# Kernel tuning notes

Measured on AMD Instinct MI355X. Metric: run time of the kernel, lower is better.

The kernel has to match this reference:

```python
import jax, jax.numpy as jnp
import numpy as np

B, SQ, SK, D, DV = 16, 2048, 2048, 64, 64
DROPOUT_P = 0.1


def setup_inputs() -> dict:
    key = jax.random.key(0)
    k1, k2, k3, k4 = jax.random.split(key, 4)
    return {
        "query": jax.random.normal(k1, (B, SQ, D), dtype=jnp.float32),
        "key": jax.random.normal(k2, (B, SK, D), dtype=jnp.float32),
        "value": jax.random.normal(k3, (B, SK, DV), dtype=jnp.float32),
        "drop_mask": jax.random.uniform(k4, (B, SQ, SK), dtype=jnp.float32),
    }


def reference(query, key, value, drop_mask):
    # scaled dot-product attention with explicit score matrix, as in the module
    scale = jnp.sqrt(jnp.asarray(key.shape[-1], dtype=query.dtype))
    qk = jnp.einsum("bqd,bkd->bqk", query, key) / scale  # [B, SQ, SK]
    attn = jax.nn.softmax(qk, axis=-1)
    # dropout: keep where uniform > p, rescale by 1/(1-p)
    keep = (drop_mask > DROPOUT_P).astype(attn.dtype)
    attn = attn * keep / (1.0 - DROPOUT_P)
    return jnp.einsum("bqk,bkv->bqv", attn, value)  # [B, SQ, DV]
```

## Files before the change

kernel.cpp:

```cpp
#include <hip/hip_runtime.h>
#include <hip/hip_bf16.h>

#define B_ 16
#define SQ_ 2048
#define SK_ 2048
#define D_ 64
#define DV_ 64
#define INV_KEEP 1.1111111f
#define QSCALE 0.1803368801f

typedef float f4 __attribute__((ext_vector_type(4)));
typedef __bf16 bf16x2 __attribute__((ext_vector_type(2)));
typedef __bf16 bf16x8 __attribute__((ext_vector_type(8)));
typedef short s16x4 __attribute__((ext_vector_type(4)));
typedef unsigned int u32;
typedef unsigned int u32x2 __attribute__((ext_vector_type(2)));
typedef unsigned int u32x4 __attribute__((ext_vector_type(4)));

static __device__ __forceinline__ unsigned short bf16u(float f) {
    u32 u = __builtin_bit_cast(u32, f);
    u += 0x7fffu + ((u >> 16) & 1u);
    return (unsigned short)(u >> 16);
}
static __device__ __forceinline__ u32 pk2(float lo, float hi) {
    return (u32)bf16u(lo) | ((u32)bf16u(hi) << 16);
}
static __device__ __forceinline__ u32 pkc(float lo, float hi) {
    bf16x2 t = {(__bf16)lo, (__bf16)hi};
    return __builtin_bit_cast(u32, t);
}

static __device__ __forceinline__ float fexp2(float x) {
#if __has_builtin(__builtin_amdgcn_exp2f)
    return __builtin_amdgcn_exp2f(x);
#else
    return exp2f(x);
#endif
}

static __device__ __forceinline__ void gload16(const void* g, void* l) {
    __builtin_amdgcn_global_load_lds(
        (const __attribute__((address_space(1))) unsigned int*)g,
        (__attribute__((address_space(3))) unsigned int*)l, 16, 0, 0);
}

template <int OFF>
static __device__ __forceinline__ f4 gload_f4(const float* p) {
    f4 d;
    if constexpr (OFF == 0)
        asm volatile("global_load_dwordx4 %0, %1, off" : "=v"(d) : "v"(p));
    else
        asm volatile("global_load_dwordx4 %0, %1, off offset:%2" : "=v"(d) : "v"(p), "i"(OFF));
    return d;
}

static __device__ __forceinline__ f4 mfma16(s16x4 a, s16x4 b, f4 c) {
#if __has_builtin(__builtin_amdgcn_mfma_f32_16x16x16bf16_1k)
    return __builtin_amdgcn_mfma_f32_16x16x16bf16_1k(a, b, c, 0, 0, 0);
#else
    f4 d;
    asm("v_mfma_f32_16x16x16_bf16 %0, %1, %2, %3" : "=v"(d) : "v"(a), "v"(b), "v"(c));
    return d;
#endif
}

__global__ __launch_bounds__(256) void kv_retile(const float* __restrict__ K,
                                                 const float* __restrict__ V,
                                                 unsigned short* __restrict__ KbT,
                                                 unsigned short* __restrict__ VtT) {
    if (blockIdx.x < 1024) {
        int b = blockIdx.x >> 6, kt = blockIdx.x & 63;
        int p = threadIdx.x;
        int s = p >> 6, g = (p >> 4) & 3, c = p & 15;
        int t = s & 1, h = s >> 1;
        const float* src = K + ((size_t)(b * SK_ + kt * 32 + 16 * t + c)) * D_ + 32 * h + 8 * g;
        f4 a = *(const f4*)src;
        f4 b2 = *(const f4*)(src + 4);
        u32x4 w;
        w[0] = pk2(a.x, a.y); w[1] = pk2(a.z, a.w);
        w[2] = pk2(b2.x, b2.y); w[3] = pk2(b2.z, b2.w);
        *(u32x4*)(KbT + ((size_t)(b * 64 + kt)) * 2048 + (size_t)p * 8) = w;
    } else {
        __shared__ float vt[32][65];
        int id = blockIdx.x - 1024;
        int b = id >> 6, kt = id & 63;
        int tid = threadIdx.x;
#pragma unroll
        for (int e = 0; e < 2; ++e) {
            int f = tid * 2 + e;
            int row = f >> 4, c4 = (f & 15) * 4;
            *(f4*)&vt[row][c4] = *(const f4*)(V + ((size_t)(b * SK_ + kt * 32 + row)) * DV_ + c4);
        }
        __syncthreads();
        int vb = tid >> 6, g = (tid >> 4) & 3, c = tid & 15;
        int v = vb * 16 + c;
        u32x4 w;
        w[0] = pk2(vt[4 * g + 0][v], vt[4 * g + 1][v]);
        w[1] = pk2(vt[4 * g + 2][v], vt[4 * g + 3][v]);
        w[2] = pk2(vt[16 + 4 * g + 0][v], vt[16 + 4 * g + 1][v]);
        w[3] = pk2(vt[16 + 4 * g + 2][v], vt[16 + 4 * g + 3][v]);
        *(u32x4*)(VtT + ((size_t)(b * 64 + kt)) * 2048 + (size_t)tid * 8) = w;
    }
}

template <int SPLIT>
__global__ __launch_bounds__(256) void attn_main(const float* __restrict__ Q,
                                                 const unsigned short* __restrict__ KbT,
                                                 const unsigned short* __restrict__ VtT,
                                                 const float* __restrict__ mask,
                                                 float* __restrict__ out,
                                                 float* __restrict__ accP,
                                                 float* __restrict__ lP) {
    constexpr int NT32 = SK_ / SPLIT / 32;
    constexpr int NB = 512 * SPLIT;
    __shared__ unsigned short sK[4][2048];
    __shared__ unsigned short sV[4][2048];

    int bswz = (blockIdx.x & 7) * (NB / 8) + (blockIdx.x >> 3);
    int wid  = threadIdx.x >> 6;
    int split = bswz & (SPLIT - 1);
    int strip = (bswz / SPLIT) * 4 + wid;
    int b  = strip >> 7;
    int q0 = (strip & 127) << 4;
    int kb = split * (SK_ / SPLIT);
    int lane = threadIdx.x & 63;
    int g = lane >> 4, c = lane & 15;

    const size_t tile0 = ((size_t)b * 64 + split * NT32) * 2048;
    const unsigned short* ksrc = KbT + tile0 + (size_t)threadIdx.x * 8;
    const unsigned short* vsrc = VtT + tile0 + (size_t)threadIdx.x * 8;
    const float* msrc = mask + ((size_t)(b * SQ_ + q0 + c)) * SK_ + kb + 4 * g;

    bf16x8 qf[2];
    {
        const float* qp = Q + ((size_t)(b * SQ_ + q0 + c)) * D_ + 8 * g;
#pragma unroll
        for (int h = 0; h < 2; ++h) {
            f4 a  = *(const f4*)(qp + h * 32);
            f4 bq = *(const f4*)(qp + h * 32 + 4);
            u32x4 wq;
            wq[0] = pk2(a.x * QSCALE, a.y * QSCALE);
            wq[1] = pk2(a.z * QSCALE, a.w * QSCALE);
            wq[2] = pk2(bq.x * QSCALE, bq.y * QSCALE);
            wq[3] = pk2(bq.z * QSCALE, bq.w * QSCALE);
            qf[h] = __builtin_bit_cast(bf16x8, wq);
        }
    }

    f4 mreg[4][2];

    auto kvload = [&](int dst, int srct) {
        gload16(ksrc + (size_t)srct * 2048, &sK[dst][wid * 512]);
        gload16(vsrc + (size_t)srct * 2048, &sV[dst][wid * 512]);
    };
    auto mload = [&](int dst, int srct) {
        const float* mp = msrc + (size_t)srct * 32;
        mreg[dst][0] = gload_f4<0>(mp);
        mreg[dst][1] = gload_f4<64>(mp);
    };

    mload(0, 0);
    kvload(0, 0); mload(1, 1);
    kvload(1, 1); mload(2, 2);
    kvload(2, 2); mload(3, 3);

    f4 acc[4];
#pragma unroll
    for (int vb = 0; vb < 4; ++vb) acc[vb] = (f4){0.f, 0.f, 0.f, 0.f};
    f4 ls0 = (f4){0.f, 0.f, 0.f, 0.f}, ls1 = (f4){0.f, 0.f, 0.f, 0.f};

    const unsigned short* kbL = &sK[0][0] + lane * 8;
    const unsigned short* vbL = &sV[0][0] + lane * 8;

#pragma unroll 4
    for (int kt = 0; kt < NT32; ++kt) {
        asm volatile("s_waitcnt vmcnt(10)" ::: "memory");
        __builtin_amdgcn_s_barrier();
        __builtin_amdgcn_sched_barrier(0);

        const int bi = kt & 3;
        const unsigned short* kB = kbL + bi * 2048;
        const unsigned short* vB = vbL + bi * 2048;

        u32x4 ka0 = *(const u32x4*)(kB);
        u32x4 ka1 = *(const u32x4*)(kB + 1024);
        u32x4 kc0 = *(const u32x4*)(kB + 512);
        u32x4 kc1 = *(const u32x4*)(kB + 1536);
        f4 st0 = (f4){0.f, 0.f, 0.f, 0.f}, st1 = (f4){0.f, 0.f, 0.f, 0.f};
        st0 = __builtin_amdgcn_mfma_f32_16x16x32_bf16(__builtin_bit_cast(bf16x8, ka0), qf[0], st0, 0, 0, 0);
        st0 = __builtin_amdgcn_mfma_f32_16x16x32_bf16(__builtin_bit_cast(bf16x8, ka1), qf[1], st0, 0, 0, 0);
        st1 = __builtin_amdgcn_mfma_f32_16x16x32_bf16(__builtin_bit_cast(bf16x8, kc0), qf[0], st1, 0, 0, 0);
        st1 = __builtin_amdgcn_mfma_f32_16x16x32_bf16(__builtin_bit_cast(bf16x8, kc1), qf[1], st1, 0, 0, 0);

        const f4 mk0 = mreg[bi][0], mk1 = mreg[bi][1];
        float pd0[4], pd1[4];
#pragma unroll
        for (int r = 0; r < 4; ++r) {
            float p0 = fexp2(st0[r]);
            ls0[r] += p0;
            pd0[r] = (mk0[r] > 0.1f) ? p0 : 0.f;
            float p1 = fexp2(st1[r]);
            ls1[r] += p1;
            pd1[r] = (mk1[r] > 0.1f) ? p1 : 0.f;
        }

        u32x2 pw0, pw1;
        pw0[0] = pkc(pd0[0], pd0[1]); pw0[1] = pkc(pd0[2], pd0[3]);
        pw1[0] = pkc(pd1[0], pd1[1]); pw1[1] = pkc(pd1[2], pd1[3]);
        s16x4 pb0 = __builtin_bit_cast(s16x4, pw0);
        s16x4 pb1 = __builtin_bit_cast(s16x4, pw1);
#pragma unroll
        for (int vb = 0; vb < 4; ++vb) {
            u32x4 vv = *(const u32x4*)(vB + vb * 512);
            u32x2 vlo, vhi;
            vlo[0] = vv[0]; vlo[1] = vv[1];
            vhi[0] = vv[2]; vhi[1] = vv[3];
            acc[vb] = mfma16(__builtin_bit_cast(s16x4, vlo), pb0, acc[vb]);
            acc[vb] = mfma16(__builtin_bit_cast(s16x4, vhi), pb1, acc[vb]);
        }

        __builtin_amdgcn_s_barrier();
        kvload((kt + 3) & 3, (kt + 3 < NT32) ? kt + 3 : NT32 - 1);
        mload((kt + 4) & 3, (kt + 4 < NT32) ? kt + 4 : NT32 - 1);
    }
    asm volatile("s_waitcnt vmcnt(0)" ::: "memory");

    float lf = ls0[0] + ls0[1] + ls0[2] + ls0[3] + ls1[0] + ls1[1] + ls1[2] + ls1[3];
    lf += __shfl_xor(lf, 16);
    lf += __shfl_xor(lf, 32);

    if constexpr (SPLIT == 1) {
        float li = INV_KEEP / lf;
        float* op = out + ((size_t)(b * SQ_ + q0 + c)) * DV_;
#pragma unroll
        for (int vb = 0; vb < 4; ++vb) {
            f4 o = acc[vb] * li;
            __builtin_nontemporal_store(o, (f4*)(op + 16 * vb + 4 * g));
        }
    } else {
        float* ap = accP + (((size_t)strip * SPLIT + split) * 64 + lane) * 16;
#pragma unroll
        for (int vb = 0; vb < 4; ++vb)
            *(f4*)(ap + 4 * vb) = acc[vb];
        if (g == 0)
            lP[((size_t)strip * SPLIT + split) * 16 + c] = lf;
    }
}

__global__ __launch_bounds__(256) void attn_combine2(const float* __restrict__ accP,
                                                     const float* __restrict__ lP,
                                                     float* __restrict__ out) {
    __shared__ float sacc[2 * 1280];
    __shared__ float sl[32];
    int strip = blockIdx.x;
    int t = threadIdx.x;
    const float* src = accP + (size_t)strip * 2048;
#pragma unroll
    for (int s = 0; s < 2; ++s)
        *(f4*)&sacc[s * 1280 + (t >> 2) * 20 + (t & 3) * 4] = *(const f4*)(src + s * 1024 + t * 4);
    if (t < 32) sl[t] = lP[(size_t)strip * 32 + t];
    __syncthreads();

    int q = t >> 4, j = t & 15;
    float L = sl[q] + sl[16 + q];
    float inv = INV_KEEP / L;
    int base = (16 * (j & 3) + q) * 20 + 4 * (j >> 2);
    f4 o = *(const f4*)&sacc[base] + *(const f4*)&sacc[1280 + base];
    o *= inv;
    int b  = strip >> 7;
    int q0 = (strip & 127) << 4;
    __builtin_nontemporal_store(o, (f4*)(out + ((size_t)(b * SQ_ + q0 + q)) * DV_ + 4 * j));
}

extern "C" void kernel_launch(void* const* d_in, const int* in_sizes, int n_in,
                              void* d_out, int out_size, void* d_ws, size_t ws_size,
                              hipStream_t stream) {
    const float* Q = (const float*)d_in[0];
    const float* K = (const float*)d_in[1];
    const float* V = (const float*)d_in[2];
    const float* M = (const float*)d_in[3];
    float* out = (float*)d_out;

    char* ws = (char*)d_ws;
    unsigned short* KbT  = (unsigned short*)ws;
    unsigned short* VtT  = (unsigned short*)(ws + (size_t)4 * 1024 * 1024);
    float*          accP = (float*)         (ws + (size_t)8 * 1024 * 1024);
    float*          lP   = (float*)         (ws + (size_t)24 * 1024 * 1024);

    const size_t need_split = (size_t)24 * 1024 * 1024 + (size_t)2048 * 2 * 16 * 4;

    kv_retile<<<2048, 256, 0, stream>>>(K, V, KbT, VtT);
    if (ws_size >= need_split) {
        attn_main<2><<<1024, 256, 0, stream>>>(Q, KbT, VtT, M, out, accP, lP);
        attn_combine2<<<2048, 256, 0, stream>>>(accP, lP, out);
    } else {
        attn_main<1><<<512, 256, 0, stream>>>(Q, KbT, VtT, M, out, nullptr, nullptr);
    }
}
```

Measured before the change: 91.25 us.

## Load K/V tiles directly into registers instead of shared LDS staging

Removes the shared-memory K/V ring buffer and the block-wide barriers. Each wave now loads its own K and V tile data straight into registers with a two-slot double buffer and a mask prefetch three tiles ahead. This drops the LDS round trip and the inter-wave synchronisation. In exchange, each of the four waves fetches the same K/V data separately, so global/L2 traffic for K/V is quadrupled and register pressure rises.

```diff
diff --git a/kernel.cpp b/kernel.cpp
--- a/kernel.cpp
+++ b/kernel.cpp
@@ -38,15 +38,18 @@
 #endif
 }
 
-static __device__ __forceinline__ void gload16(const void* g, void* l) {
-    __builtin_amdgcn_global_load_lds(
-        (const __attribute__((address_space(1))) unsigned int*)g,
-        (__attribute__((address_space(3))) unsigned int*)l, 16, 0, 0);
-}
-
 template <int OFF>
 static __device__ __forceinline__ f4 gload_f4(const float* p) {
     f4 d;
+    if constexpr (OFF == 0)
+        asm volatile("global_load_dwordx4 %0, %1, off" : "=v"(d) : "v"(p));
+    else
+        asm volatile("global_load_dwordx4 %0, %1, off offset:%2" : "=v"(d) : "v"(p), "i"(OFF));
+    return d;
+}
+template <int OFF>
+static __device__ __forceinline__ u32x4 gload_u4(const unsigned short* p) {
+    u32x4 d;
     if constexpr (OFF == 0)
         asm volatile("global_load_dwordx4 %0, %1, off" : "=v"(d) : "v"(p));
     else
@@ -113,8 +116,6 @@
                                                  float* __restrict__ lP) {
     constexpr int NT32 = SK_ / SPLIT / 32;
     constexpr int NB = 512 * SPLIT;
-    __shared__ unsigned short sK[4][2048];
-    __shared__ unsigned short sV[4][2048];
 
     int bswz = (blockIdx.x & 7) * (NB / 8) + (blockIdx.x >> 3);
     int wid  = threadIdx.x >> 6;
@@ -127,8 +128,8 @@
     int g = lane >> 4, c = lane & 15;
 
     const size_t tile0 = ((size_t)b * 64 + split * NT32) * 2048;
-    const unsigned short* ksrc = KbT + tile0 + (size_t)threadIdx.x * 8;
-    const unsigned short* vsrc = VtT + tile0 + (size_t)threadIdx.x * 8;
+    const unsigned short* ksrc = KbT + tile0 + (size_t)lane * 8;
+    const unsigned short* vsrc = VtT + tile0 + (size_t)lane * 8;
     const float* msrc = mask + ((size_t)(b * SQ_ + q0 + c)) * SK_ + kb + 4 * g;
 
     bf16x8 qf[2];
@@ -146,53 +147,56 @@
             qf[h] = __builtin_bit_cast(bf16x8, wq);
         }
     }
-
-    f4 mreg[4][2];
-
-    auto kvload = [&](int dst, int srct) {
-        gload16(ksrc + (size_t)srct * 2048, &sK[dst][wid * 512]);
-        gload16(vsrc + (size_t)srct * 2048, &sV[dst][wid * 512]);
+    __builtin_amdgcn_sched_barrier(0);
+
+    u32x4 kr[2][4];
+    u32x4 vr[2][4];
+    f4    mr[4][2];
+
+    auto kvload = [&](int slot, int srct) {
+        const unsigned short* kp = ksrc + (size_t)srct * 2048;
+        kr[slot][0] = gload_u4<0>(kp);
+        kr[slot][1] = gload_u4<1024>(kp);
+        kr[slot][2] = gload_u4<2048>(kp);
+        kr[slot][3] = gload_u4<3072>(kp);
+        const unsigned short* vp = vsrc + (size_t)srct * 2048;
+        vr[slot][0] = gload_u4<0>(vp);
+        vr[slot][1] = gload_u4<1024>(vp);
+        vr[slot][2] = gload_u4<2048>(vp);
+        vr[slot][3] = gload_u4<3072>(vp);
     };
-    auto mload = [&](int dst, int srct) {
+    auto mload = [&](int slot, int srct) {
         const float* mp = msrc + (size_t)srct * 32;
-        mreg[dst][0] = gload_f4<0>(mp);
-        mreg[dst][1] = gload_f4<64>(mp);
+        mr[slot][0] = gload_f4<0>(mp);
+        mr[slot][1] = gload_f4<64>(mp);
     };
 
     mload(0, 0);
-    kvload(0, 0); mload(1, 1);
-    kvload(1, 1); mload(2, 2);
-    kvload(2, 2); mload(3, 3);
+    mload(1, 1);
+    kvload(0, 0);
+    mload(2, 2);
 
     f4 acc[4];
 #pragma unroll
     for (int vb = 0; vb < 4; ++vb) acc[vb] = (f4){0.f, 0.f, 0.f, 0.f};
     f4 ls0 = (f4){0.f, 0.f, 0.f, 0.f}, ls1 = (f4){0.f, 0.f, 0.f, 0.f};
 
-    const unsigned short* kbL = &sK[0][0] + lane * 8;
-    const unsigned short* vbL = &sV[0][0] + lane * 8;
-
 #pragma unroll 4
     for (int kt = 0; kt < NT32; ++kt) {
-        asm volatile("s_waitcnt vmcnt(10)" ::: "memory");
-        __builtin_amdgcn_s_barrier();
+        kvload((kt + 1) & 1, (kt + 1 < NT32) ? kt + 1 : NT32 - 1);
+        mload((kt + 3) & 3, (kt + 3 < NT32) ? kt + 3 : NT32 - 1);
+        asm volatile("s_waitcnt vmcnt(12)" ::: "memory");
         __builtin_amdgcn_sched_barrier(0);
 
-        const int bi = kt & 3;
-        const unsigned short* kB = kbL + bi * 2048;
-        const unsigned short* vB = vbL + bi * 2048;
-
-        u32x4 ka0 = *(const u32x4*)(kB);
-        u32x4 ka1 = *(const u32x4*)(kB + 1024);
-        u32x4 kc0 = *(const u32x4*)(kB + 512);
-        u32x4 kc1 = *(const u32x4*)(kB + 1536);
+        const int ks = kt & 1, ms = kt & 3;
+
         f4 st0 = (f4){0.f, 0.f, 0.f, 0.f}, st1 = (f4){0.f, 0.f, 0.f, 0.f};
-        st0 = __builtin_amdgcn_mfma_f32_16x16x32_bf16(__builtin_bit_cast(bf16x8, ka0), qf[0], st0, 0, 0, 0);
-        st0 = __builtin_amdgcn_mfma_f32_16x16x32_bf16(__builtin_bit_cast(bf16x8, ka1), qf[1], st0, 0, 0, 0);
-        st1 = __builtin_amdgcn_mfma_f32_16x16x32_bf16(__builtin_bit_cast(bf16x8, kc0), qf[0], st1, 0, 0, 0);
-        st1 = __builtin_amdgcn_mfma_f32_16x16x32_bf16(__builtin_bit_cast(bf16x8, kc1), qf[1], st1, 0, 0, 0);
-
-        const f4 mk0 = mreg[bi][0], mk1 = mreg[bi][1];
+        st0 = __builtin_amdgcn_mfma_f32_16x16x32_bf16(__builtin_bit_cast(bf16x8, kr[ks][0]), qf[0], st0, 0, 0, 0);
+        st0 = __builtin_amdgcn_mfma_f32_16x16x32_bf16(__builtin_bit_cast(bf16x8, kr[ks][2]), qf[1], st0, 0, 0, 0);
+        st1 = __builtin_amdgcn_mfma_f32_16x16x32_bf16(__builtin_bit_cast(bf16x8, kr[ks][1]), qf[0], st1, 0, 0, 0);
+        st1 = __builtin_amdgcn_mfma_f32_16x16x32_bf16(__builtin_bit_cast(bf16x8, kr[ks][3]), qf[1], st1, 0, 0, 0);
+
+        const f4 mk0 = mr[ms][0], mk1 = mr[ms][1];
         float pd0[4], pd1[4];
 #pragma unroll
         for (int r = 0; r < 4; ++r) {
@@ -211,19 +215,16 @@
         s16x4 pb1 = __builtin_bit_cast(s16x4, pw1);
 #pragma unroll
         for (int vb = 0; vb < 4; ++vb) {
-            u32x4 vv = *(const u32x4*)(vB + vb * 512);
+            u32x4 vv = vr[ks][vb];
             u32x2 vlo, vhi;
             vlo[0] = vv[0]; vlo[1] = vv[1];
             vhi[0] = vv[2]; vhi[1] = vv[3];
             acc[vb] = mfma16(__builtin_bit_cast(s16x4, vlo), pb0, acc[vb]);
             acc[vb] = mfma16(__builtin_bit_cast(s16x4, vhi), pb1, acc[vb]);
         }
-
-        __builtin_amdgcn_s_barrier();
-        kvload((kt + 3) & 3, (kt + 3 < NT32) ? kt + 3 : NT32 - 1);
-        mload((kt + 4) & 3, (kt + 4 < NT32) ? kt + 4 : NT32 - 1);
     }
     asm volatile("s_waitcnt vmcnt(0)" ::: "memory");
+    __builtin_amdgcn_sched_barrier(0);
 
     float lf = ls0[0] + ls0[1] + ls0[2] + ls0[3] + ls1[0] + ls1[1] + ls1[2] + ls1[3];
     lf += __shfl_xor(lf, 16);
```

New measurement: 105.4 us. +15.5%, slower.

## Split keys four ways with a shallower pipeline to raise occupancy

Applied to the files above, without the earlier changes.

Moves from a 2-way to a 4-way key split (2048 blocks) and adds a combine kernel that sums four partials. LDS ring buffers shrink from 4 to 2 stages and the mask prefetch shrinks from 4 register sets to one, with launch_bounds(256,7) added so more waves fit per CU. The goal is more latency hiding through more resident waves and blocks. The cost is less prefetch depth for the mask stream, which dominates memory traffic, plus twice the partial-accumulator traffic and a heavier combine step.

```diff
diff --git a/kernel.cpp b/kernel.cpp
--- a/kernel.cpp
+++ b/kernel.cpp
@@ -29,7 +29,6 @@
     bf16x2 t = {(__bf16)lo, (__bf16)hi};
     return __builtin_bit_cast(u32, t);
 }
-
 static __device__ __forceinline__ float fexp2(float x) {
 #if __has_builtin(__builtin_amdgcn_exp2f)
     return __builtin_amdgcn_exp2f(x);
@@ -37,13 +36,11 @@
     return exp2f(x);
 #endif
 }
-
 static __device__ __forceinline__ void gload16(const void* g, void* l) {
     __builtin_amdgcn_global_load_lds(
         (const __attribute__((address_space(1))) unsigned int*)g,
         (__attribute__((address_space(3))) unsigned int*)l, 16, 0, 0);
 }
-
 template <int OFF>
 static __device__ __forceinline__ f4 gload_f4(const float* p) {
     f4 d;
@@ -53,7 +50,6 @@
         asm volatile("global_load_dwordx4 %0, %1, off offset:%2" : "=v"(d) : "v"(p), "i"(OFF));
     return d;
 }
-
 static __device__ __forceinline__ f4 mfma16(s16x4 a, s16x4 b, f4 c) {
 #if __has_builtin(__builtin_amdgcn_mfma_f32_16x16x16bf16_1k)
     return __builtin_amdgcn_mfma_f32_16x16x16bf16_1k(a, b, c, 0, 0, 0);
@@ -104,17 +100,17 @@
 }
 
 template <int SPLIT>
-__global__ __launch_bounds__(256) void attn_main(const float* __restrict__ Q,
-                                                 const unsigned short* __restrict__ KbT,
-                                                 const unsigned short* __restrict__ VtT,
-                                                 const float* __restrict__ mask,
-                                                 float* __restrict__ out,
-                                                 float* __restrict__ accP,
-                                                 float* __restrict__ lP) {
+__global__ __launch_bounds__(256, 7) void attn_main(const float* __restrict__ Q,
+                                                    const unsigned short* __restrict__ KbT,
+                                                    const unsigned short* __restrict__ VtT,
+                                                    const float* __restrict__ mask,
+                                                    float* __restrict__ out,
+                                                    float* __restrict__ accP,
+                                                    float* __restrict__ lP) {
     constexpr int NT32 = SK_ / SPLIT / 32;
     constexpr int NB = 512 * SPLIT;
-    __shared__ unsigned short sK[4][2048];
-    __shared__ unsigned short sV[4][2048];
+    __shared__ unsigned short sK[2][2048];
+    __shared__ unsigned short sV[2][2048];
 
     int bswz = (blockIdx.x & 7) * (NB / 8) + (blockIdx.x >> 3);
     int wid  = threadIdx.x >> 6;
@@ -146,62 +142,66 @@
             qf[h] = __builtin_bit_cast(bf16x8, wq);
         }
     }
-
-    f4 mreg[4][2];
+    __builtin_amdgcn_sched_barrier(0);
 
     auto kvload = [&](int dst, int srct) {
         gload16(ksrc + (size_t)srct * 2048, &sK[dst][wid * 512]);
         gload16(vsrc + (size_t)srct * 2048, &sV[dst][wid * 512]);
     };
-    auto mload = [&](int dst, int srct) {
-        const float* mp = msrc + (size_t)srct * 32;
-        mreg[dst][0] = gload_f4<0>(mp);
-        mreg[dst][1] = gload_f4<64>(mp);
-    };
-
-    mload(0, 0);
-    kvload(0, 0); mload(1, 1);
-    kvload(1, 1); mload(2, 2);
-    kvload(2, 2); mload(3, 3);
+
+    f4 mka, mkb;
+    mka = gload_f4<0>(msrc);
+    mkb = gload_f4<64>(msrc);
+    kvload(0, 0);
+    kvload(1, 1);
 
     f4 acc[4];
 #pragma unroll
     for (int vb = 0; vb < 4; ++vb) acc[vb] = (f4){0.f, 0.f, 0.f, 0.f};
-    f4 ls0 = (f4){0.f, 0.f, 0.f, 0.f}, ls1 = (f4){0.f, 0.f, 0.f, 0.f};
+    float lf = 0.f;
 
     const unsigned short* kbL = &sK[0][0] + lane * 8;
     const unsigned short* vbL = &sV[0][0] + lane * 8;
 
 #pragma unroll 4
     for (int kt = 0; kt < NT32; ++kt) {
-        asm volatile("s_waitcnt vmcnt(10)" ::: "memory");
+        asm volatile("s_waitcnt vmcnt(2)" ::: "memory");
         __builtin_amdgcn_s_barrier();
         __builtin_amdgcn_sched_barrier(0);
 
-        const int bi = kt & 3;
+        const int bi = kt & 1;
         const unsigned short* kB = kbL + bi * 2048;
         const unsigned short* vB = vbL + bi * 2048;
 
-        u32x4 ka0 = *(const u32x4*)(kB);
-        u32x4 ka1 = *(const u32x4*)(kB + 1024);
-        u32x4 kc0 = *(const u32x4*)(kB + 512);
-        u32x4 kc1 = *(const u32x4*)(kB + 1536);
         f4 st0 = (f4){0.f, 0.f, 0.f, 0.f}, st1 = (f4){0.f, 0.f, 0.f, 0.f};
-        st0 = __builtin_amdgcn_mfma_f32_16x16x32_bf16(__builtin_bit_cast(bf16x8, ka0), qf[0], st0, 0, 0, 0);
-        st0 = __builtin_amdgcn_mfma_f32_16x16x32_bf16(__builtin_bit_cast(bf16x8, ka1), qf[1], st0, 0, 0, 0);
-        st1 = __builtin_amdgcn_mfma_f32_16x16x32_bf16(__builtin_bit_cast(bf16x8, kc0), qf[0], st1, 0, 0, 0);
-        st1 = __builtin_amdgcn_mfma_f32_16x16x32_bf16(__builtin_bit_cast(bf16x8, kc1), qf[1], st1, 0, 0, 0);
-
-        const f4 mk0 = mreg[bi][0], mk1 = mreg[bi][1];
+        {
+            u32x4 ka = *(const u32x4*)(kB);
+            u32x4 kc = *(const u32x4*)(kB + 512);
+            st0 = __builtin_amdgcn_mfma_f32_16x16x32_bf16(__builtin_bit_cast(bf16x8, ka), qf[0], st0, 0, 0, 0);
+            st1 = __builtin_amdgcn_mfma_f32_16x16x32_bf16(__builtin_bit_cast(bf16x8, kc), qf[0], st1, 0, 0, 0);
+        }
+        {
+            u32x4 ka = *(const u32x4*)(kB + 1024);
+            u32x4 kc = *(const u32x4*)(kB + 1536);
+            st0 = __builtin_amdgcn_mfma_f32_16x16x32_bf16(__builtin_bit_cast(bf16x8, ka), qf[1], st0, 0, 0, 0);
+            st1 = __builtin_amdgcn_mfma_f32_16x16x32_bf16(__builtin_bit_cast(bf16x8, kc), qf[1], st1, 0, 0, 0);
+        }
+
         float pd0[4], pd1[4];
 #pragma unroll
         for (int r = 0; r < 4; ++r) {
             float p0 = fexp2(st0[r]);
-            ls0[r] += p0;
-            pd0[r] = (mk0[r] > 0.1f) ? p0 : 0.f;
+            lf += p0;
+            pd0[r] = (mka[r] > 0.1f) ? p0 : 0.f;
             float p1 = fexp2(st1[r]);
-            ls1[r] += p1;
-            pd1[r] = (mk1[r] > 0.1f) ? p1 : 0.f;
+            lf += p1;
+            pd1[r] = (mkb[r] > 0.1f) ? p1 : 0.f;
+        }
+
+        {
+            const float* mp = msrc + (size_t)((kt + 1 < NT32) ? kt + 1 : NT32 - 1) * 32;
+            mka = gload_f4<0>(mp);
+            mkb = gload_f4<64>(mp);
         }
 
         u32x2 pw0, pw1;
@@ -220,12 +220,12 @@
         }
 
         __builtin_amdgcn_s_barrier();
-        kvload((kt + 3) & 3, (kt + 3 < NT32) ? kt + 3 : NT32 - 1);
-        mload((kt + 4) & 3, (kt + 4 < NT32) ? kt + 4 : NT32 - 1);
+        __builtin_amdgcn_sched_barrier(0);
+        kvload(bi, (kt + 2 < NT32) ? kt + 2 : NT32 - 1);
     }
     asm volatile("s_waitcnt vmcnt(0)" ::: "memory");
-
-    float lf = ls0[0] + ls0[1] + ls0[2] + ls0[3] + ls1[0] + ls1[1] + ls1[2] + ls1[3];
+    __builtin_amdgcn_sched_barrier(0);
+
     lf += __shfl_xor(lf, 16);
     lf += __shfl_xor(lf, 32);
 
@@ -247,25 +247,28 @@
     }
 }
 
-__global__ __launch_bounds__(256) void attn_combine2(const float* __restrict__ accP,
+__global__ __launch_bounds__(256) void attn_combine4(const float* __restrict__ accP,
                                                      const float* __restrict__ lP,
                                                      float* __restrict__ out) {
-    __shared__ float sacc[2 * 1280];
-    __shared__ float sl[32];
+    __shared__ float sacc[4 * 1280];
+    __shared__ float sl[64];
     int strip = blockIdx.x;
     int t = threadIdx.x;
-    const float* src = accP + (size_t)strip * 2048;
-#pragma unroll
-    for (int s = 0; s < 2; ++s)
+    const float* src = accP + (size_t)strip * 4096;
+#pragma unroll
+    for (int s = 0; s < 4; ++s)
         *(f4*)&sacc[s * 1280 + (t >> 2) * 20 + (t & 3) * 4] = *(const f4*)(src + s * 1024 + t * 4);
-    if (t < 32) sl[t] = lP[(size_t)strip * 32 + t];
+    if (t < 64) sl[t] = lP[(size_t)strip * 64 + t];
     __syncthreads();
 
     int q = t >> 4, j = t & 15;
-    float L = sl[q] + sl[16 + q];
+    float L = sl[q] + sl[16 + q] + sl[32 + q] + sl[48 + q];
     float inv = INV_KEEP / L;
     int base = (16 * (j & 3) + q) * 20 + 4 * (j >> 2);
-    f4 o = *(const f4*)&sacc[base] + *(const f4*)&sacc[1280 + base];
+    f4 o = (f4){0.f, 0.f, 0.f, 0.f};
+#pragma unroll
+    for (int s = 0; s < 4; ++s)
+        o += *(const f4*)&sacc[s * 1280 + base];
     o *= inv;
     int b  = strip >> 7;
     int q0 = (strip & 127) << 4;
@@ -285,14 +288,14 @@
     unsigned short* KbT  = (unsigned short*)ws;
     unsigned short* VtT  = (unsigned short*)(ws + (size_t)4 * 1024 * 1024);
     float*          accP = (float*)         (ws + (size_t)8 * 1024 * 1024);
-    float*          lP   = (float*)         (ws + (size_t)24 * 1024 * 1024);
-
-    const size_t need_split = (size_t)24 * 1024 * 1024 + (size_t)2048 * 2 * 16 * 4;
+    float*          lP   = (float*)         (ws + (size_t)40 * 1024 * 1024);
+
+    const size_t need_split = (size_t)40 * 1024 * 1024 + (size_t)2048 * 4 * 16 * 4;
 
     kv_retile<<<2048, 256, 0, stream>>>(K, V, KbT, VtT);
     if (ws_size >= need_split) {
-        attn_main<2><<<1024, 256, 0, stream>>>(Q, KbT, VtT, M, out, accP, lP);
-        attn_combine2<<<2048, 256, 0, stream>>>(accP, lP, out);
+        attn_main<4><<<2048, 256, 0, stream>>>(Q, KbT, VtT, M, out, accP, lP);
+        attn_combine4<<<2048, 256, 0, stream>>>(accP, lP, out);
     } else {
         attn_main<1><<<512, 256, 0, stream>>>(Q, KbT, VtT, M, out, nullptr, nullptr);
     }
```

Measured after the change: 105.2 us. 15.3% more time.

## Switch attention main loop to 64-key double-buffered steps with MFMA priority

Applied to the files above, without the earlier changes.

The main loop now processes 64 keys per iteration using two shared-memory buffers of 4096 elements, in place of a four-deep ring of 32-key tiles. K/V and mask prefetch run two steps ahead. The point is to halve the number of barriers and waitcnts per key and to batch more MFMAs per iteration. s_setprio is raised around the MFMA sections so the scheduler favours matrix work. The cost is a shallower pipeline, with only one step of lookahead in flight, and higher register use for the mask and score tiles.

```diff
diff --git a/kernel.cpp b/kernel.cpp
--- a/kernel.cpp
+++ b/kernel.cpp
@@ -29,7 +29,6 @@
     bf16x2 t = {(__bf16)lo, (__bf16)hi};
     return __builtin_bit_cast(u32, t);
 }
-
 static __device__ __forceinline__ float fexp2(float x) {
 #if __has_builtin(__builtin_amdgcn_exp2f)
     return __builtin_amdgcn_exp2f(x);
@@ -37,13 +36,11 @@
     return exp2f(x);
 #endif
 }
-
 static __device__ __forceinline__ void gload16(const void* g, void* l) {
     __builtin_amdgcn_global_load_lds(
         (const __attribute__((address_space(1))) unsigned int*)g,
         (__attribute__((address_space(3))) unsigned int*)l, 16, 0, 0);
 }
-
 template <int OFF>
 static __device__ __forceinline__ f4 gload_f4(const float* p) {
     f4 d;
@@ -53,7 +50,6 @@
         asm volatile("global_load_dwordx4 %0, %1, off offset:%2" : "=v"(d) : "v"(p), "i"(OFF));
     return d;
 }
-
 static __device__ __forceinline__ f4 mfma16(s16x4 a, s16x4 b, f4 c) {
 #if __has_builtin(__builtin_amdgcn_mfma_f32_16x16x16bf16_1k)
     return __builtin_amdgcn_mfma_f32_16x16x16bf16_1k(a, b, c, 0, 0, 0);
@@ -111,10 +107,10 @@
                                                  float* __restrict__ out,
                                                  float* __restrict__ accP,
                                                  float* __restrict__ lP) {
-    constexpr int NT32 = SK_ / SPLIT / 32;
+    constexpr int NT64 = SK_ / SPLIT / 64;
     constexpr int NB = 512 * SPLIT;
-    __shared__ unsigned short sK[4][2048];
-    __shared__ unsigned short sV[4][2048];
+    __shared__ unsigned short sK[2][4096];
+    __shared__ unsigned short sV[2][4096];
 
     int bswz = (blockIdx.x & 7) * (NB / 8) + (blockIdx.x >> 3);
     int wid  = threadIdx.x >> 6;
@@ -126,7 +122,7 @@
     int lane = threadIdx.x & 63;
     int g = lane >> 4, c = lane & 15;
 
-    const size_t tile0 = ((size_t)b * 64 + split * NT32) * 2048;
+    const size_t tile0 = ((size_t)b * 64 + split * (SK_ / SPLIT / 32)) * 2048;
     const unsigned short* ksrc = KbT + tile0 + (size_t)threadIdx.x * 8;
     const unsigned short* vsrc = VtT + tile0 + (size_t)threadIdx.x * 8;
     const float* msrc = mask + ((size_t)(b * SQ_ + q0 + c)) * SK_ + kb + 4 * g;
@@ -146,23 +142,28 @@
             qf[h] = __builtin_bit_cast(bf16x8, wq);
         }
     }
-
-    f4 mreg[4][2];
-
-    auto kvload = [&](int dst, int srct) {
-        gload16(ksrc + (size_t)srct * 2048, &sK[dst][wid * 512]);
-        gload16(vsrc + (size_t)srct * 2048, &sV[dst][wid * 512]);
+    __builtin_amdgcn_sched_barrier(0);
+
+    f4 mr[2][4];
+
+    auto kvload = [&](int buf, int st) {
+        const unsigned short* kp = ksrc + (size_t)st * 4096;
+        gload16(kp,        &sK[buf][wid * 512]);
+        gload16(kp + 2048, &sK[buf][2048 + wid * 512]);
+        const unsigned short* vp = vsrc + (size_t)st * 4096;
+        gload16(vp,        &sV[buf][wid * 512]);
+        gload16(vp + 2048, &sV[buf][2048 + wid * 512]);
     };
-    auto mload = [&](int dst, int srct) {
-        const float* mp = msrc + (size_t)srct * 32;
-        mreg[dst][0] = gload_f4<0>(mp);
-        mreg[dst][1] = gload_f4<64>(mp);
+    auto mload = [&](int buf, int st) {
+        const float* mp = msrc + (size_t)st * 64;
+        mr[buf][0] = gload_f4<0>(mp);
+        mr[buf][1] = gload_f4<64>(mp);
+        mr[buf][2] = gload_f4<128>(mp);
+        mr[buf][3] = gload_f4<192>(mp);
     };
 
-    mload(0, 0);
-    kvload(0, 0); mload(1, 1);
-    kvload(1, 1); mload(2, 2);
-    kvload(2, 2); mload(3, 3);
+    kvload(0, 0); mload(0, 0);
+    kvload(1, 1); mload(1, 1);
 
     f4 acc[4];
 #pragma unroll
@@ -173,57 +174,77 @@
     const unsigned short* vbL = &sV[0][0] + lane * 8;
 
 #pragma unroll 4
-    for (int kt = 0; kt < NT32; ++kt) {
-        asm volatile("s_waitcnt vmcnt(10)" ::: "memory");
+    for (int st = 0; st < NT64; ++st) {
+        asm volatile("s_waitcnt vmcnt(8)" ::: "memory");
         __builtin_amdgcn_s_barrier();
         __builtin_amdgcn_sched_barrier(0);
 
-        const int bi = kt & 3;
-        const unsigned short* kB = kbL + bi * 2048;
-        const unsigned short* vB = vbL + bi * 2048;
-
-        u32x4 ka0 = *(const u32x4*)(kB);
-        u32x4 ka1 = *(const u32x4*)(kB + 1024);
-        u32x4 kc0 = *(const u32x4*)(kB + 512);
-        u32x4 kc1 = *(const u32x4*)(kB + 1536);
-        f4 st0 = (f4){0.f, 0.f, 0.f, 0.f}, st1 = (f4){0.f, 0.f, 0.f, 0.f};
-        st0 = __builtin_amdgcn_mfma_f32_16x16x32_bf16(__builtin_bit_cast(bf16x8, ka0), qf[0], st0, 0, 0, 0);
-        st0 = __builtin_amdgcn_mfma_f32_16x16x32_bf16(__builtin_bit_cast(bf16x8, ka1), qf[1], st0, 0, 0, 0);
-        st1 = __builtin_amdgcn_mfma_f32_16x16x32_bf16(__builtin_bit_cast(bf16x8, kc0), qf[0], st1, 0, 0, 0);
-        st1 = __builtin_amdgcn_mfma_f32_16x16x32_bf16(__builtin_bit_cast(bf16x8, kc1), qf[1], st1, 0, 0, 0);
-
-        const f4 mk0 = mreg[bi][0], mk1 = mreg[bi][1];
-        float pd0[4], pd1[4];
-#pragma unroll
-        for (int r = 0; r < 4; ++r) {
-            float p0 = fexp2(st0[r]);
-            ls0[r] += p0;
-            pd0[r] = (mk0[r] > 0.1f) ? p0 : 0.f;
-            float p1 = fexp2(st1[r]);
-            ls1[r] += p1;
-            pd1[r] = (mk1[r] > 0.1f) ? p1 : 0.f;
-        }
-
-        u32x2 pw0, pw1;
-        pw0[0] = pkc(pd0[0], pd0[1]); pw0[1] = pkc(pd0[2], pd0[3]);
-        pw1[0] = pkc(pd1[0], pd1[1]); pw1[1] = pkc(pd1[2], pd1[3]);
-        s16x4 pb0 = __builtin_bit_cast(s16x4, pw0);
-        s16x4 pb1 = __builtin_bit_cast(s16x4, pw1);
-#pragma unroll
-        for (int vb = 0; vb < 4; ++vb) {
-            u32x4 vv = *(const u32x4*)(vB + vb * 512);
-            u32x2 vlo, vhi;
-            vlo[0] = vv[0]; vlo[1] = vv[1];
-            vhi[0] = vv[2]; vhi[1] = vv[3];
-            acc[vb] = mfma16(__builtin_bit_cast(s16x4, vlo), pb0, acc[vb]);
-            acc[vb] = mfma16(__builtin_bit_cast(s16x4, vhi), pb1, acc[vb]);
-        }
+        const int buf = st & 1;
+        const unsigned short* kB = kbL + buf * 4096;
+        const unsigned short* vB = vbL + buf * 4096;
+
+        f4 stt[4];
+        __builtin_amdgcn_s_setprio(1);
+#pragma unroll
+        for (int h = 0; h < 2; ++h) {
+            u32x4 k0 = *(const u32x4*)(kB + h * 2048);
+            u32x4 k1 = *(const u32x4*)(kB + h * 2048 + 512);
+            u32x4 k2 = *(const u32x4*)(kB + h * 2048 + 1024);
+            u32x4 k3 = *(const u32x4*)(kB + h * 2048 + 1536);
+            f4 s0 = (f4){0.f, 0.f, 0.f, 0.f}, s1 = (f4){0.f, 0.f, 0.f, 0.f};
+            s0 = __builtin_amdgcn_mfma_f32_16x16x32_bf16(__builtin_bit_cast(bf16x8, k0), qf[0], s0, 0, 0, 0);
+            s0 = __builtin_amdgcn_mfma_f32_16x16x32_bf16(__builtin_bit_cast(bf16x8, k2), qf[1], s0, 0, 0, 0);
+            s1 = __builtin_amdgcn_mfma_f32_16x16x32_bf16(__builtin_bit_cast(bf16x8, k1), qf[0], s1, 0, 0, 0);
+            s1 = __builtin_amdgcn_mfma_f32_16x16x32_bf16(__builtin_bit_cast(bf16x8, k3), qf[1], s1, 0, 0, 0);
+            stt[h * 2]     = s0;
+            stt[h * 2 + 1] = s1;
+        }
+        __builtin_amdgcn_s_setprio(0);
+
+        float pd[4][4];
+#pragma unroll
+        for (int j = 0; j < 4; ++j) {
+            const f4 mk = mr[buf][j];
+#pragma unroll
+            for (int r = 0; r < 4; ++r) {
+                float p = fexp2(stt[j][r]);
+                if (j & 1) ls1[r] += p; else ls0[r] += p;
+                pd[j][r] = (mk[r] > 0.1f) ? p : 0.f;
+            }
+        }
+
+        __builtin_amdgcn_s_setprio(1);
+#pragma unroll
+        for (int h = 0; h < 2; ++h) {
+            u32x2 pw0, pw1;
+            pw0[0] = pkc(pd[h * 2][0], pd[h * 2][1]);
+            pw0[1] = pkc(pd[h * 2][2], pd[h * 2][3]);
+            pw1[0] = pkc(pd[h * 2 + 1][0], pd[h * 2 + 1][1]);
+            pw1[1] = pkc(pd[h * 2 + 1][2], pd[h * 2 + 1][3]);
+            s16x4 pb0 = __builtin_bit_cast(s16x4, pw0);
+            s16x4 pb1 = __builtin_bit_cast(s16x4, pw1);
+#pragma unroll
+            for (int vb = 0; vb < 4; ++vb) {
+                u32x4 vv = *(const u32x4*)(vB + h * 2048 + vb * 512);
+                u32x2 vlo, vhi;
+                vlo[0] = vv[0]; vlo[1] = vv[1];
+                vhi[0] = vv[2]; vhi[1] = vv[3];
+                acc[vb] = mfma16(__builtin_bit_cast(s16x4, vlo), pb0, acc[vb]);
+                acc[vb] = mfma16(__builtin_bit_cast(s16x4, vhi), pb1, acc[vb]);
+            }
+        }
+        __builtin_amdgcn_s_setprio(0);
 
         __builtin_amdgcn_s_barrier();
-        kvload((kt + 3) & 3, (kt + 3 < NT32) ? kt + 3 : NT32 - 1);
-        mload((kt + 4) & 3, (kt + 4 < NT32) ? kt + 4 : NT32 - 1);
+        __builtin_amdgcn_sched_barrier(0);
+        {
+            const int nt = (st + 2 < NT64) ? st + 2 : NT64 - 1;
+            kvload(buf, nt);
+            mload(buf, nt);
+        }
     }
     asm volatile("s_waitcnt vmcnt(0)" ::: "memory");
+    __builtin_amdgcn_sched_barrier(0);
 
     float lf = ls0[0] + ls0[1] + ls0[2] + ls0[3] + ls1[0] + ls1[1] + ls1[2] + ls1[3];
     lf += __shfl_xor(lf, 16);
```

After: 90.34 us. No clear change (-1.0%).
